# Performance work log

Hardware: AMD Instinct MI355X
Metric: run time of the kernel (lower is better)

Reference implementation:

```python
import jax, jax.numpy as jnp
import numpy as np

M, N, D, P = 1024, 1024, 64, 4096
H = N // D
L = P + M  # total KV length


def setup_inputs() -> dict:
    key = jax.random.key(0)
    ks = jax.random.split(key, 7)
    s = 1.0 / np.float32(np.sqrt(N))
    return {
        "X": jax.random.normal(ks[0], (M, N), jnp.float32),
        "W_q": jax.random.normal(ks[1], (N, N), jnp.float32) * s,
        "W_k": jax.random.normal(ks[2], (N, N), jnp.float32) * s,
        "W_v": jax.random.normal(ks[3], (N, N), jnp.float32) * s,
        "cache_K": jax.random.normal(ks[4], (H, P, D), jnp.float32),
        "cache_V": jax.random.normal(ks[5], (H, P, D), jnp.float32),
        "noise": jax.random.normal(ks[6], (H, M, L), jnp.float32) * 0.5,
    }


def reference(X, W_q, W_k, W_v, cache_K, cache_V, noise):
    # Projections: [M, N] -> [M, H, D]
    q = (X @ W_q).reshape(M, H, D)
    k = (X @ W_k).reshape(M, H, D).transpose(1, 0, 2)  # [H, M, D]
    v = (X @ W_v).reshape(M, H, D).transpose(1, 0, 2)  # [H, M, D]

    # KV cache concat (HND layout): [H, L, D]
    k_cache = jnp.concatenate([cache_K, k], axis=1)
    v_cache = jnp.concatenate([cache_V, v], axis=1)

    # Full QK^T scores, sm_scale=1.0, non-causal (flashinfer default): [H, M, L]
    scores = jnp.einsum("mhd,hld->hml", q, k_cache)
    weights = jax.nn.softmax(scores, axis=-1)  # == flash-attention probs (sm_scale=1.0)

    # Attention output: [M, H, D] -> [M, N]
    output = jnp.einsum("hml,hld->mhd", weights, v_cache).reshape(M, N)

    # Keyformer noise-perturbed importance softmax (temperature 1.5): [H, M, L]
    perturb_out = jax.nn.softmax((scores + noise) / 1.5, axis=-1)

    return output, weights, perturb_out
```

## Files before the change

### kernel.cpp

```cpp
#include <hip/hip_runtime.h>
#include <stdint.h>

#define MM 1024
#define NN 1024
#define DD 64
#define PP 4096
#define HH 16
#define LL 5120
#define SHC 12.0f

typedef float  f32x4  __attribute__((ext_vector_type(4)));
typedef short  s16x8  __attribute__((ext_vector_type(8)));
typedef short  s16x4  __attribute__((ext_vector_type(4)));
typedef __bf16 bf16x8 __attribute__((ext_vector_type(8)));

static __device__ __forceinline__ unsigned short f2bf(float f) {
    unsigned u = __float_as_uint(f);
    u += 0x7FFFu + ((u >> 16) & 1u);
    return (unsigned short)(u >> 16);
}
static __device__ __forceinline__ float bf2f(unsigned short h) {
    return __uint_as_float(((unsigned)h) << 16);
}
static __device__ __forceinline__ f32x4 mfma16(s16x8 a, s16x8 b, f32x4 c) {
    return __builtin_amdgcn_mfma_f32_16x16x32_bf16(
        __builtin_bit_cast(bf16x8, a), __builtin_bit_cast(bf16x8, b), c, 0, 0, 0);
}

__global__ void k_prep(const float* __restrict__ X, const float* __restrict__ cK,
                       unsigned short* __restrict__ Xh, unsigned short* __restrict__ Xl,
                       unsigned short* __restrict__ Kall) {
    const int nX4 = (MM * NN) / 4;
    const int nK4 = (HH * PP * DD) / 4;
    int stride = gridDim.x * blockDim.x;
    for (int i = blockIdx.x * blockDim.x + threadIdx.x; i < nX4 + nK4; i += stride) {
        if (i < nX4) {
            f32x4 v = reinterpret_cast<const f32x4*>(X)[i];
            s16x4 h, l;
            for (int j = 0; j < 4; ++j) {
                float f = v[j];
                unsigned short hb = f2bf(f);
                h[j] = (short)hb;
                l[j] = (short)f2bf(f - bf2f(hb));
            }
            reinterpret_cast<s16x4*>(Xh)[i] = h;
            reinterpret_cast<s16x4*>(Xl)[i] = l;
        } else {
            int j = i - nX4;
            f32x4 v = reinterpret_cast<const f32x4*>(cK)[j];
            s16x4 h;
            for (int jj = 0; jj < 4; ++jj) h[jj] = (short)f2bf(v[jj]);
            int e = j * 4;
            int hh = e >> 18;
            int rem = e & 262143;
            int64_t de = (int64_t)hh * (LL * DD) + rem;
            *reinterpret_cast<s16x4*>(Kall + de) = h;
        }
    }
}

__global__ void k_transW(const float* __restrict__ Wq, const float* __restrict__ Wk,
                         const float* __restrict__ Wv,
                         unsigned short* __restrict__ WhT, unsigned short* __restrict__ WlT) {
    __shared__ float t[64][68];
    int z = blockIdx.z;
    const float* W = (z == 0) ? Wq : ((z == 1) ? Wk : Wv);
    int n0 = blockIdx.x * 64, k0 = blockIdx.y * 64;
    int tc = threadIdx.x & 15, tr = threadIdx.x >> 4;
    for (int i = 0; i < 4; ++i) {
        int r = tr + i * 16;
        f32x4 v = *reinterpret_cast<const f32x4*>(W + (int64_t)(k0 + r) * NN + n0 + tc * 4);
        t[r][tc * 4 + 0] = v[0]; t[r][tc * 4 + 1] = v[1];
        t[r][tc * 4 + 2] = v[2]; t[r][tc * 4 + 3] = v[3];
    }
    __syncthreads();
    int64_t zoff = (int64_t)z * MM * NN;
    for (int i = 0; i < 4; ++i) {
        int rr = tr + i * 16;
        s16x4 h, l;
        for (int j = 0; j < 4; ++j) {
            float f = t[tc * 4 + j][rr];
            unsigned short hb = f2bf(f);
            h[j] = (short)hb;
            l[j] = (short)f2bf(f - bf2f(hb));
        }
        *reinterpret_cast<s16x4*>(WhT + zoff + (int64_t)(n0 + rr) * NN + k0 + tc * 4) = h;
        *reinterpret_cast<s16x4*>(WlT + zoff + (int64_t)(n0 + rr) * NN + k0 + tc * 4) = l;
    }
}

__launch_bounds__(256, 4)
__global__ void k_gemm(const unsigned short* __restrict__ Xh, const unsigned short* __restrict__ Xl,
                       const unsigned short* __restrict__ WhT, const unsigned short* __restrict__ WlT,
                       unsigned short* __restrict__ Qh, unsigned short* __restrict__ Ql,
                       unsigned short* __restrict__ Kall, unsigned short* __restrict__ Vproj) {
    __shared__ unsigned short sb[2 * 64 * 72];
    unsigned short* As = sb;
    unsigned short* Bs = sb + 64 * 72;
    int z = blockIdx.z;
    int n0 = blockIdx.x * 64, m0 = blockIdx.y * 64;
    int tid = threadIdx.x, lane = tid & 63, wave = tid >> 6;
    int lrow = lane & 15, lgrp = lane >> 4;
    int wm = (wave >> 1) * 32, wn = (wave & 1) * 32;
    f32x4 acc[2][2] = {};
    for (int seg = 0; seg < 3; ++seg) {
        const unsigned short* Asrc = (seg == 2) ? Xl : Xh;
        const unsigned short* Bsrc = ((seg == 1) ? WlT : WhT) + (int64_t)z * MM * NN;
        for (int kt = 0; kt < 16; ++kt) {
            int kb = kt * 64;
            for (int i = 0; i < 2; ++i) {
                int idx = i * 256 + tid;
                int r = idx >> 3, c8 = (idx & 7) * 8;
                *reinterpret_cast<s16x8*>(&As[r * 72 + c8]) =
                    *reinterpret_cast<const s16x8*>(Asrc + (int64_t)(m0 + r) * NN + kb + c8);
                *reinterpret_cast<s16x8*>(&Bs[r * 72 + c8]) =
                    *reinterpret_cast<const s16x8*>(Bsrc + (int64_t)(n0 + r) * NN + kb + c8);
            }
            __syncthreads();
            for (int ks = 0; ks < 2; ++ks) {
                s16x8 af[2], bfr[2];
                for (int f = 0; f < 2; ++f)
                    af[f] = *reinterpret_cast<const s16x8*>(&As[(wm + f * 16 + lrow) * 72 + ks * 32 + lgrp * 8]);
                for (int f = 0; f < 2; ++f)
                    bfr[f] = *reinterpret_cast<const s16x8*>(&Bs[(wn + f * 16 + lrow) * 72 + ks * 32 + lgrp * 8]);
                for (int i = 0; i < 2; ++i)
                    for (int j = 0; j < 2; ++j)
                        acc[i][j] = mfma16(af[i], bfr[j], acc[i][j]);
            }
            __syncthreads();
        }
    }
    unsigned short* Cs = sb;
    auto stageC = [&](int lo) {
        for (int i = 0; i < 2; ++i)
            for (int j = 0; j < 2; ++j)
                for (int r = 0; r < 4; ++r) {
                    float v = acc[i][j][r];
                    unsigned short hv = f2bf(v);
                    if (lo) hv = f2bf(v - bf2f(hv));
                    Cs[(wm + i * 16 + lgrp * 4 + r) * 72 + wn + j * 16 + lrow] = hv;
                }
    };
    auto writeC = [&](unsigned short* dst, int kmode) {
        for (int i = 0; i < 2; ++i) {
            int idx = i * 256 + tid;
            int r = idx >> 3, c8 = (idx & 7) * 8;
            s16x8 v = *reinterpret_cast<const s16x8*>(&Cs[r * 72 + c8]);
            int gm = m0 + r, gn = n0 + c8;
            if (kmode) {
                int hh = gn >> 6, d = gn & 63;
                *reinterpret_cast<s16x8*>(dst + ((int64_t)hh * LL + PP + gm) * DD + d) = v;
            } else {
                *reinterpret_cast<s16x8*>(dst + (int64_t)gm * NN + gn) = v;
            }
        }
    };
    __syncthreads();
    if (z == 0) {
        stageC(0); __syncthreads(); writeC(Qh, 0);
        __syncthreads(); stageC(1); __syncthreads(); writeC(Ql, 0);
    } else if (z == 1) {
        stageC(0); __syncthreads(); writeC(Kall, 1);
    } else {
        stageC(0); __syncthreads(); writeC(Vproj, 0);
    }
}

__global__ void k_transV(const float* __restrict__ cV, const unsigned short* __restrict__ Vproj,
                         unsigned short* __restrict__ VT) {
    __shared__ unsigned short Ts[64][72];
    int b = blockIdx.x;
    int hh = b / 80, lt = b % 80;
    int l0 = lt * 64;
    int tid = threadIdx.x;
    if (l0 < PP) {
        for (int i = 0; i < 4; ++i) {
            int idx = i * 256 + tid;
            int r = idx >> 4, c4 = (idx & 15) * 4;
            f32x4 v = *reinterpret_cast<const f32x4*>(cV + ((int64_t)hh * PP + l0 + r) * DD + c4);
            s16x4 o;
            for (int j = 0; j < 4; ++j) o[j] = (short)f2bf(v[j]);
            *reinterpret_cast<s16x4*>(&Ts[r][c4]) = o;
        }
    } else {
        for (int i = 0; i < 2; ++i) {
            int idx = i * 256 + tid;
            int r = idx >> 3, c8 = (idx & 7) * 8;
            *reinterpret_cast<s16x8*>(&Ts[r][c8]) =
                *reinterpret_cast<const s16x8*>(Vproj + (int64_t)(l0 - PP + r) * NN + hh * DD + c8);
        }
    }
    __syncthreads();
    for (int i = 0; i < 2; ++i) {
        int idx = i * 256 + tid;
        int d = idx >> 3, l8 = (idx & 7) * 8;
        s16x8 v;
        for (int j = 0; j < 8; ++j) v[j] = (short)Ts[l8 + j][d];
        *reinterpret_cast<s16x8*>(VT + ((int64_t)hh * DD + d) * LL + l0 + l8) = v;
    }
}

__launch_bounds__(256, 4)
__global__ void k_attn2(const unsigned short* __restrict__ Qh, const unsigned short* __restrict__ Ql,
                        const unsigned short* __restrict__ Kall, const unsigned short* __restrict__ VT,
                        const float* __restrict__ noise,
                        float* __restrict__ outO, float* __restrict__ outW, float* __restrict__ outP) {
    __shared__ float sc[16][276];
    __shared__ unsigned short wls[16][264];
    __shared__ float sred[4][16][2];
    __shared__ float siwp[16][2];

    int id = blockIdx.x;
    int xcd = id & 7, j = id >> 3;
    int hh = xcd * 2 + (j >> 6);
    int mt = j & 63;
    int m0 = mt * 16;
    int tid = threadIdx.x, lane = tid & 63, wave = tid >> 6;
    int lrow = lane & 15, lgrp = lane >> 4;
    int erow = tid >> 4, cb = tid & 15;

    s16x8 aqh[2], aql[2];
    for (int ks = 0; ks < 2; ++ks) {
        int64_t off = (int64_t)(m0 + lrow) * NN + hh * DD + ks * 32 + lgrp * 8;
        aqh[ks] = *reinterpret_cast<const s16x8*>(Qh + off);
        aql[ks] = *reinterpret_cast<const s16x8*>(Ql + off);
    }
    const unsigned short* Kh = Kall + (int64_t)hh * LL * DD;
    const unsigned short* Vh = VT + (int64_t)hh * DD * LL;
    const float* nzw = noise + ((int64_t)hh * MM + m0) * LL;
    const float* nzr = nzw + (int64_t)erow * LL;
    float* Wr = outW + ((int64_t)hh * MM + m0 + erow) * LL;
    float* Pr = outP + ((int64_t)hh * MM + m0 + erow) * LL;

    float Sw4[4] = {}, Sp4[4] = {};
    for (int c = 0; c < 20; ++c) {
        int c0 = c * 256;
        int lb = c0 + wave * 64;
        float nzv[4][4];
        for (int r = 0; r < 4; ++r)
            for (int lf = 0; lf < 4; ++lf)
                nzv[r][lf] = nzw[(int64_t)(lgrp * 4 + r) * LL + lb + lf * 16 + lrow];
        f32x4 sacc[4] = {};
        for (int ks = 0; ks < 2; ++ks)
            for (int lf = 0; lf < 4; ++lf) {
                s16x8 bk = *reinterpret_cast<const s16x8*>(
                    Kh + (int64_t)(lb + lf * 16 + lrow) * DD + ks * 32 + lgrp * 8);
                sacc[lf] = mfma16(aqh[ks], bk, sacc[lf]);
                sacc[lf] = mfma16(aql[ks], bk, sacc[lf]);
            }
        for (int lf = 0; lf < 4; ++lf)
            for (int r = 0; r < 4; ++r) {
                float s = sacc[lf][r];
                Sw4[r] += __expf(s - SHC);
                Sp4[r] += __expf((s + nzv[r][lf]) * (1.f / 1.5f) - SHC);
            }
    }
    for (int r = 0; r < 4; ++r)
        for (int d = 1; d < 16; d <<= 1) {
            Sw4[r] += __shfl_xor(Sw4[r], d, 64);
            Sp4[r] += __shfl_xor(Sp4[r], d, 64);
        }
    if (lrow == 0)
        for (int r = 0; r < 4; ++r) {
            sred[wave][lgrp * 4 + r][0] = Sw4[r];
            sred[wave][lgrp * 4 + r][1] = Sp4[r];
        }
    __syncthreads();
    if (tid < 32) {
        int row = tid >> 1, ty = tid & 1;
        float S = sred[0][row][ty] + sred[1][row][ty] + sred[2][row][ty] + sred[3][row][ty];
        siwp[row][ty] = 1.f / S;
    }
    __syncthreads();
    float iw = siwp[erow][0], ip = siwp[erow][1];

    f32x4 oacc[4] = {};
    for (int c = 19; c >= 0; --c) {
        int c0 = c * 256;
        s16x8 vv[4];
        for (int df = 0; df < 4; ++df)
            vv[df] = *reinterpret_cast<const s16x8*>(
                Vh + (int64_t)(df * 16 + lrow) * LL + c0 + wave * 64 + lgrp * 8);
        f32x4 nv[4];
        for (int q = 0; q < 4; ++q)
            nv[q] = *reinterpret_cast<const f32x4*>(nzr + c0 + q * 64 + cb * 4);
        {
            f32x4 sacc[4] = {};
            int lb = c0 + wave * 64;
            for (int ks = 0; ks < 2; ++ks)
                for (int lf = 0; lf < 4; ++lf) {
                    s16x8 bk = *reinterpret_cast<const s16x8*>(
                        Kh + (int64_t)(lb + lf * 16 + lrow) * DD + ks * 32 + lgrp * 8);
                    sacc[lf] = mfma16(aqh[ks], bk, sacc[lf]);
                    sacc[lf] = mfma16(aql[ks], bk, sacc[lf]);
                }
            for (int lf = 0; lf < 4; ++lf)
                for (int r = 0; r < 4; ++r)
                    sc[lgrp * 4 + r][wave * 64 + lf * 16 + lrow] = sacc[lf][r];
        }
        __syncthreads();
        for (int q = 0; q < 4; ++q) {
            int col = q * 64 + cb * 4;
            f32x4 s = *reinterpret_cast<const f32x4*>(&sc[erow][col]);
            f32x4 wv, pv;
            for (int jj = 0; jj < 4; ++jj) {
                wv[jj] = __expf(s[jj] - SHC) * iw;
                pv[jj] = __expf((s[jj] + nv[q][jj]) * (1.f / 1.5f) - SHC) * ip;
            }
            *reinterpret_cast<f32x4*>(Wr + c0 + col) = wv;
            *reinterpret_cast<f32x4*>(Pr + c0 + col) = pv;
            s16x4 pk;
            for (int jj = 0; jj < 4; ++jj) pk[jj] = (short)f2bf(wv[jj]);
            *reinterpret_cast<s16x4*>(&wls[erow][col]) = pk;
        }
        __syncthreads();
        {
            int k0 = wave * 64;
            s16x8 bw0 = *reinterpret_cast<const s16x8*>(&wls[lrow][k0 + lgrp * 8]);
            for (int df = 0; df < 4; ++df)
                oacc[df] = mfma16(vv[df], bw0, oacc[df]);
            s16x8 bw1 = *reinterpret_cast<const s16x8*>(&wls[lrow][k0 + 32 + lgrp * 8]);
            for (int df = 0; df < 4; ++df) {
                s16x8 av = *reinterpret_cast<const s16x8*>(
                    Vh + (int64_t)(df * 16 + lrow) * LL + c0 + k0 + 32 + lgrp * 8);
                oacc[df] = mfma16(av, bw1, oacc[df]);
            }
        }
    }
    __syncthreads();
    float* ored = &sc[0][0];
    for (int df = 0; df < 4; ++df)
        for (int r = 0; r < 4; ++r)
            ored[(wave * 64 + df * 16 + lgrp * 4 + r) * 17 + lrow] = oacc[df][r];
    __syncthreads();
    for (int i = 0; i < 4; ++i) {
        int idx = i * 256 + tid;
        int m = idx >> 6, d = idx & 63;
        float v = ored[d * 17 + m] + ored[(64 + d) * 17 + m] +
                  ored[(128 + d) * 17 + m] + ored[(192 + d) * 17 + m];
        outO[(int64_t)(m0 + m) * NN + hh * DD + d] = v;
    }
}

extern "C" void kernel_launch(void* const* d_in, const int* in_sizes, int n_in,
                              void* d_out, int out_size, void* d_ws, size_t ws_size,
                              hipStream_t stream) {
    const float* X  = (const float*)d_in[0];
    const float* Wq = (const float*)d_in[1];
    const float* Wk = (const float*)d_in[2];
    const float* Wv = (const float*)d_in[3];
    const float* cK = (const float*)d_in[4];
    const float* cV = (const float*)d_in[5];
    const float* nz = (const float*)d_in[6];

    char* ws = (char*)d_ws;
    const int64_t U = 1 << 21;
    unsigned short* Xh    = (unsigned short*)(ws + 0 * U);
    unsigned short* Xl    = (unsigned short*)(ws + 1 * U);
    unsigned short* WhT   = (unsigned short*)(ws + 2 * U);
    unsigned short* WlT   = (unsigned short*)(ws + 5 * U);
    unsigned short* Qh    = (unsigned short*)(ws + 8 * U);
    unsigned short* Ql    = (unsigned short*)(ws + 9 * U);
    unsigned short* Kall  = (unsigned short*)(ws + 10 * U);
    unsigned short* Vproj = (unsigned short*)(ws + 15 * U);
    unsigned short* VT    = (unsigned short*)(ws + 16 * U);

    float* outO = (float*)d_out;
    float* outW = outO + (int64_t)MM * NN;
    float* outP = outW + (int64_t)HH * MM * LL;

    k_prep<<<2048, 256, 0, stream>>>(X, cK, Xh, Xl, Kall);
    k_transW<<<dim3(16, 16, 3), 256, 0, stream>>>(Wq, Wk, Wv, WhT, WlT);
    k_gemm<<<dim3(16, 16, 3), 256, 0, stream>>>(Xh, Xl, WhT, WlT, Qh, Ql, Kall, Vproj);
    k_transV<<<1280, 256, 0, stream>>>(cV, Vproj, VT);
    k_attn2<<<1024, 256, 0, stream>>>(Qh, Ql, Kall, VT, nz, outO, outW, outP);
}
```

Baseline: 531.6 us.

## Make second attention pass wave-private to drop block barriers

The second pass now has each wave compute softmax weights straight from its MFMA accumulator fragments and stage its own bf16 weight tile in a per-wave double-buffered LDS slot. This removes the shared score tile and the two block-wide barriers per chunk. The cost is that W and P outputs are written as scattered per-lane scalar stores instead of coalesced float4 row stores, which may raise global write transaction overhead. Noise is also read in fragment layout rather than as vectorised rows.

New measurement: 548.9 us. 3.3% more time.

```diff
diff --git a/kernel.cpp b/kernel.cpp
--- a/kernel.cpp
+++ b/kernel.cpp
@@ -205,8 +205,7 @@
                         const unsigned short* __restrict__ Kall, const unsigned short* __restrict__ VT,
                         const float* __restrict__ noise,
                         float* __restrict__ outO, float* __restrict__ outW, float* __restrict__ outP) {
-    __shared__ float sc[16][276];
-    __shared__ unsigned short wls[16][264];
+    __shared__ __align__(16) char smem[18432];
     __shared__ float sred[4][16][2];
     __shared__ float siwp[16][2];
 
@@ -217,7 +216,6 @@
     int m0 = mt * 16;
     int tid = threadIdx.x, lane = tid & 63, wave = tid >> 6;
     int lrow = lane & 15, lgrp = lane >> 4;
-    int erow = tid >> 4, cb = tid & 15;
 
     s16x8 aqh[2], aql[2];
     for (int ks = 0; ks < 2; ++ks) {
@@ -228,14 +226,10 @@
     const unsigned short* Kh = Kall + (int64_t)hh * LL * DD;
     const unsigned short* Vh = VT + (int64_t)hh * DD * LL;
     const float* nzw = noise + ((int64_t)hh * MM + m0) * LL;
-    const float* nzr = nzw + (int64_t)erow * LL;
-    float* Wr = outW + ((int64_t)hh * MM + m0 + erow) * LL;
-    float* Pr = outP + ((int64_t)hh * MM + m0 + erow) * LL;
 
     float Sw4[4] = {}, Sp4[4] = {};
     for (int c = 0; c < 20; ++c) {
-        int c0 = c * 256;
-        int lb = c0 + wave * 64;
+        int lb = c * 256 + wave * 64;
         float nzv[4][4];
         for (int r = 0; r < 4; ++r)
             for (int lf = 0; lf < 4; ++lf)
@@ -272,63 +266,54 @@
         siwp[row][ty] = 1.f / S;
     }
     __syncthreads();
-    float iw = siwp[erow][0], ip = siwp[erow][1];
-
+    float iwr[4], ipr[4];
+    for (int r = 0; r < 4; ++r) {
+        iwr[r] = siwp[lgrp * 4 + r][0];
+        ipr[r] = siwp[lgrp * 4 + r][1];
+    }
+
+    typedef unsigned short wls_t[2][16][72];
+    wls_t* wls = (wls_t*)smem;
+    float* Wb = outW + ((int64_t)hh * MM + m0) * LL;
+    float* Pb = outP + ((int64_t)hh * MM + m0) * LL;
     f32x4 oacc[4] = {};
     for (int c = 19; c >= 0; --c) {
-        int c0 = c * 256;
-        s16x8 vv[4];
-        for (int df = 0; df < 4; ++df)
-            vv[df] = *reinterpret_cast<const s16x8*>(
-                Vh + (int64_t)(df * 16 + lrow) * LL + c0 + wave * 64 + lgrp * 8);
-        f32x4 nv[4];
-        for (int q = 0; q < 4; ++q)
-            nv[q] = *reinterpret_cast<const f32x4*>(nzr + c0 + q * 64 + cb * 4);
-        {
-            f32x4 sacc[4] = {};
-            int lb = c0 + wave * 64;
-            for (int ks = 0; ks < 2; ++ks)
-                for (int lf = 0; lf < 4; ++lf) {
-                    s16x8 bk = *reinterpret_cast<const s16x8*>(
-                        Kh + (int64_t)(lb + lf * 16 + lrow) * DD + ks * 32 + lgrp * 8);
-                    sacc[lf] = mfma16(aqh[ks], bk, sacc[lf]);
-                    sacc[lf] = mfma16(aql[ks], bk, sacc[lf]);
-                }
+        int lb = c * 256 + wave * 64;
+        float nfr[4][4];
+        for (int r = 0; r < 4; ++r)
             for (int lf = 0; lf < 4; ++lf)
-                for (int r = 0; r < 4; ++r)
-                    sc[lgrp * 4 + r][wave * 64 + lf * 16 + lrow] = sacc[lf][r];
-        }
-        __syncthreads();
-        for (int q = 0; q < 4; ++q) {
-            int col = q * 64 + cb * 4;
-            f32x4 s = *reinterpret_cast<const f32x4*>(&sc[erow][col]);
-            f32x4 wv, pv;
-            for (int jj = 0; jj < 4; ++jj) {
-                wv[jj] = __expf(s[jj] - SHC) * iw;
-                pv[jj] = __expf((s[jj] + nv[q][jj]) * (1.f / 1.5f) - SHC) * ip;
-            }
-            *reinterpret_cast<f32x4*>(Wr + c0 + col) = wv;
-            *reinterpret_cast<f32x4*>(Pr + c0 + col) = pv;
-            s16x4 pk;
-            for (int jj = 0; jj < 4; ++jj) pk[jj] = (short)f2bf(wv[jj]);
-            *reinterpret_cast<s16x4*>(&wls[erow][col]) = pk;
-        }
-        __syncthreads();
-        {
-            int k0 = wave * 64;
-            s16x8 bw0 = *reinterpret_cast<const s16x8*>(&wls[lrow][k0 + lgrp * 8]);
-            for (int df = 0; df < 4; ++df)
-                oacc[df] = mfma16(vv[df], bw0, oacc[df]);
-            s16x8 bw1 = *reinterpret_cast<const s16x8*>(&wls[lrow][k0 + 32 + lgrp * 8]);
+                nfr[r][lf] = nzw[(int64_t)(lgrp * 4 + r) * LL + lb + lf * 16 + lrow];
+        f32x4 sacc[4] = {};
+        for (int ks = 0; ks < 2; ++ks)
+            for (int lf = 0; lf < 4; ++lf) {
+                s16x8 bk = *reinterpret_cast<const s16x8*>(
+                    Kh + (int64_t)(lb + lf * 16 + lrow) * DD + ks * 32 + lgrp * 8);
+                sacc[lf] = mfma16(aqh[ks], bk, sacc[lf]);
+                sacc[lf] = mfma16(aql[ks], bk, sacc[lf]);
+            }
+        unsigned short (*wb)[72] = wls[wave][c & 1];
+        for (int lf = 0; lf < 4; ++lf)
+            for (int r = 0; r < 4; ++r) {
+                float s = sacc[lf][r];
+                float wv = __expf(s - SHC) * iwr[r];
+                float pv = __expf((s + nfr[r][lf]) * (1.f / 1.5f) - SHC) * ipr[r];
+                int row = lgrp * 4 + r;
+                int64_t eoff = (int64_t)row * LL + lb + lf * 16 + lrow;
+                Wb[eoff] = wv;
+                Pb[eoff] = pv;
+                wb[row][lf * 16 + lrow] = f2bf(wv);
+            }
+        for (int ks = 0; ks < 2; ++ks) {
+            s16x8 bw = *reinterpret_cast<const s16x8*>(&wb[lrow][ks * 32 + lgrp * 8]);
             for (int df = 0; df < 4; ++df) {
                 s16x8 av = *reinterpret_cast<const s16x8*>(
-                    Vh + (int64_t)(df * 16 + lrow) * LL + c0 + k0 + 32 + lgrp * 8);
-                oacc[df] = mfma16(av, bw1, oacc[df]);
-            }
-        }
-    }
-    __syncthreads();
-    float* ored = &sc[0][0];
+                    Vh + (int64_t)(df * 16 + lrow) * LL + lb + ks * 32 + lgrp * 8);
+                oacc[df] = mfma16(av, bw, oacc[df]);
+            }
+        }
+    }
+    __syncthreads();
+    float* ored = (float*)smem;
     for (int df = 0; df < 4; ++df)
         for (int r = 0; r < 4; ++r)
             ored[(wave * 64 + df * 16 + lgrp * 4 + r) * 17 + lrow] = oacc[df][r];
```
